# Kernel tuning notes

Measured on AMD Instinct MI355X. Metric: run time of the kernel, lower is better.

## Reference

```python
import jax, jax.numpy as jnp
import numpy as np

B, SQ, SK, D, H, DK, DV = 4, 2048, 2048, 1024, 16, 64, 64


def setup_inputs() -> dict:
    key = jax.random.key(0)
    ks = jax.random.split(key, 12)

    def xav(k, shape):
        fan_in, fan_out = shape[-2], shape[-1]
        lim = (6.0 / (fan_in + fan_out)) ** 0.5
        return jax.random.uniform(k, shape, jnp.float32, -lim, lim)

    return {
        "Q": jax.random.normal(ks[0], (B, SQ, D), jnp.float32),
        "K": jax.random.normal(ks[1], (B, SK, D), jnp.float32),
        "V": jax.random.normal(ks[2], (B, SK, D), jnp.float32),
        "padding_mask": jnp.zeros((B, 1, SK), jnp.bool_),
        "Wq": xav(ks[3], (H, D, DK)),
        "bq": jnp.zeros((H, DK), jnp.float32),
        "Wk": xav(ks[4], (H, D, DK)),
        "bk": jnp.zeros((H, DK), jnp.float32),
        "Wv": xav(ks[5], (H, D, DV)),
        "bv": jnp.zeros((H, DV), jnp.float32),
        "Wo": xav(ks[6], (H, DV, DV)),   # per-head Attention.linear
        "bo": jnp.zeros((H, DV), jnp.float32),
        "Wf": xav(ks[7], (H * DV, D)),   # final MultiHeadAttention.linear
        "bf": jnp.zeros((D,), jnp.float32),
    }


def reference(Q, K, V, padding_mask, Wq, bq, Wk, bk, Wv, bv, Wo, bo, Wf, bf):
    # Per-head projections, batched over heads instead of a python loop.
    q = jnp.einsum("bsd,hdk->bhsk", Q, Wq) + bq[:, None, :]  # [B,H,SQ,DK]
    k = jnp.einsum("bsd,hdk->bhsk", K, Wk) + bk[:, None, :]  # [B,H,SK,DK]
    v = jnp.einsum("bsd,hdv->bhsv", V, Wv) + bv[:, None, :]  # [B,H,SK,DV]

    scale = float(DK) ** 0.5
    w = jnp.einsum("bhqd,bhkd->bhqk", q, k) / scale           # [B,H,SQ,SK]

    causal = jnp.triu(jnp.ones((SQ, SK), jnp.bool_), 1)       # masking=True path
    w = jnp.where(causal[None, None], -jnp.inf, w)
    w = jnp.where(padding_mask[:, None, :, :], -jnp.inf, w)   # [B,1,1,SK]

    score = jnp.nan_to_num(jax.nn.softmax(w, axis=-1))        # nan_to_num as in torch
    # dropout p=0.0 -> identity
    ctx = jnp.einsum("bhqk,bhkv->bhqv", score, v)             # [B,H,SQ,DV]
    heads = jnp.einsum("bhqv,hvu->bhqu", ctx, Wo) + bo[:, None, :]
    concat = heads.transpose(0, 2, 1, 3).reshape(B, SQ, H * DV)
    return concat @ Wf + bf
```

## Files before the change

kernel.cpp:

```cpp
#include <hip/hip_runtime.h>

typedef unsigned short u16;
typedef unsigned int u32;
typedef __attribute__((ext_vector_type(8))) short short8;
typedef __attribute__((ext_vector_type(4))) float f32x4;

#define NEG (-1e30f)
#define SCL 0.180336880f

#define WS_WPQ   (0u)
#define WS_WPK   (2u<<20)
#define WS_WPV   (4u<<20)
#define WS_WBIG  (6u<<20)
#define WS_BC    (8u<<20)
#define WS_MB    ((8u<<20)+(1u<<16))
#define WS_MP    ((8u<<20)+(3u<<16))
#define WS_QB    (9u<<20)
#define WS_KB    (25u<<20)
#define WS_VB    (41u<<20)
#define WS_QP    (57u<<20)
#define WS_KP    (73u<<20)
#define WS_VP    (89u<<20)
#define WS_VT    (105u<<20)
#define WS_CTX   (121u<<20)

__device__ __forceinline__ u16 f2b(float f) {
    union { float f; unsigned u; } x; x.f = f;
    unsigned r = x.u + 0x7fffu + ((x.u >> 16) & 1u);
    return (u16)(r >> 16);
}

__device__ __forceinline__ u32 cvt_pk(float a, float b) {
    u32 r;
    asm("v_cvt_pk_bf16_f32 %0, %1, %2" : "=v"(r) : "v"(a), "v"(b));
    return r;
}

__device__ __forceinline__ void gload16(const void* g, void* lds) {
    __builtin_amdgcn_global_load_lds(
        (const __attribute__((address_space(1))) void*)g,
        (__attribute__((address_space(3))) void*)lds, 16, 0, 0);
}

__global__ __launch_bounds__(256) void conv_bf16(const float* __restrict__ in,
                                                 u16* __restrict__ out) {
    unsigned i = blockIdx.x * 256u + threadIdx.x;
    const float4* p = (const float4*)(in + (size_t)i * 8);
    float4 a = p[0], b = p[1];
    short8 o;
    o[0]=(short)f2b(a.x); o[1]=(short)f2b(a.y); o[2]=(short)f2b(a.z); o[3]=(short)f2b(a.w);
    o[4]=(short)f2b(b.x); o[5]=(short)f2b(b.y); o[6]=(short)f2b(b.z); o[7]=(short)f2b(b.w);
    *(short8*)(out + (size_t)i * 8) = o;
}

__global__ __launch_bounds__(256) void pack_qkv(const float* __restrict__ Wq,
                                                const float* __restrict__ Wk,
                                                const float* __restrict__ Wv,
                                                u16* __restrict__ pq,
                                                u16* __restrict__ pk,
                                                u16* __restrict__ pv) {
    __shared__ u16 T[64][68];
    const int dt = blockIdx.x, h = blockIdx.y;
    const int r = threadIdx.x >> 2, c0 = (threadIdx.x & 3) * 16;
    const float* srcs[3] = {Wq, Wk, Wv};
    u16* dsts[3] = {pq, pk, pv};
#pragma unroll
    for (int m = 0; m < 3; ++m) {
        const float* src = srcs[m] + (size_t)(h * 1024 + dt * 64 + r) * 64 + c0;
#pragma unroll
        for (int i4 = 0; i4 < 4; ++i4) {
            float4 x = *(const float4*)(src + i4 * 4);
            T[c0 + i4*4 + 0][r] = f2b(x.x);
            T[c0 + i4*4 + 1][r] = f2b(x.y);
            T[c0 + i4*4 + 2][r] = f2b(x.z);
            T[c0 + i4*4 + 3][r] = f2b(x.w);
        }
        __syncthreads();
        u16* dst = dsts[m] + (size_t)(h * 64 + r) * 1024 + dt * 64 + c0;
        short8 o0, o1;
#pragma unroll
        for (int i = 0; i < 8; ++i) { o0[i] = (short)T[r][c0 + i]; o1[i] = (short)T[r][c0 + 8 + i]; }
        *(short8*)dst = o0;
        *(short8*)(dst + 8) = o1;
        __syncthreads();
    }
}

__global__ __launch_bounds__(256) void make_wbig(const float* __restrict__ Wo,
                                                 const float* __restrict__ Wf,
                                                 u16* __restrict__ wbig) {
    __shared__ float WoL[64][64];
    const int ct = blockIdx.x, h = blockIdx.y;
    const int tid = threadIdx.x;
#pragma unroll
    for (int r = 0; r < 16; ++r) {
        int i = r * 256 + tid;
        WoL[i >> 6][i & 63] = Wo[h * 4096 + i];
    }
    __syncthreads();
    const int n = ct * 256 + tid;
    float wf[64];
#pragma unroll
    for (int u = 0; u < 64; ++u)
        wf[u] = Wf[(size_t)(h * 64 + u) * 1024 + n];
    u16* dst = wbig + (size_t)n * 1024 + h * 64;
    for (int vb = 0; vb < 64; vb += 8) {
        short8 o;
#pragma unroll
        for (int t = 0; t < 8; ++t) {
            int v = vb + t;
            float s = 0.f;
#pragma unroll
            for (int u4 = 0; u4 < 16; ++u4) {
                float4 w4 = *(const float4*)&WoL[v][u4 * 4];
                s += w4.x * wf[u4*4] + w4.y * wf[u4*4+1] + w4.z * wf[u4*4+2] + w4.w * wf[u4*4+3];
            }
            o[t] = (short)f2b(s);
        }
        *(short8*)(dst + vb) = o;
    }
}

__global__ __launch_bounds__(256) void make_bcomb(const float* __restrict__ bo,
                                                  const float* __restrict__ bf,
                                                  const float* __restrict__ Wf,
                                                  const unsigned char* __restrict__ pmask,
                                                  float* __restrict__ bc,
                                                  float* __restrict__ mbias,
                                                  int* __restrict__ mpart) {
    __shared__ float red[16][17];
    const int tx = threadIdx.x & 15, ty = threadIdx.x >> 4;
    const int n = blockIdx.x * 16 + tx;
    float s = 0.f;
#pragma unroll
    for (int i = 0; i < 64; ++i) {
        int x = ty * 64 + i;
        s += bo[x] * Wf[(size_t)x * 1024 + n];
    }
    red[ty][tx] = s;

    int t = blockIdx.x * 256 + threadIdx.x;
    int v = 0;
    if (t < 8192) {
        v = pmask[t] ? 1 : 0;
        mbias[t] = v ? NEG : 0.f;
    }
    int ba = __syncthreads_or(v);
    if (threadIdx.x == 0 && blockIdx.x < 32) mpart[blockIdx.x] = ba;

    if (ty == 0) {
        float tt = bf[n];
#pragma unroll
        for (int y = 0; y < 16; ++y) tt += red[y][tx];
        bc[n] = tt;
    }
}

__global__ __launch_bounds__(256) void vtrans(const u16* __restrict__ vp,
                                              u16* __restrict__ vt) {
    const int kvt = blockIdx.x, bh = blockIdx.y, b = bh >> 4, h = bh & 15;
    const int tid = threadIdx.x;
    __shared__ u16 T[64][72];
    {
        int kv_r = tid >> 2, dg = (tid & 3) * 16;
        const u16* src = vp + ((size_t)(b * 2048 + kvt * 64 + kv_r)) * 1024 + h * 64 + dg;
        short8 x0 = *(const short8*)src;
        short8 x1 = *(const short8*)(src + 8);
#pragma unroll
        for (int i = 0; i < 8; ++i) { T[dg + i][kv_r] = (u16)x0[i]; T[dg + 8 + i][kv_r] = (u16)x1[i]; }
    }
    __syncthreads();
    {
        int dv = tid >> 2, cg = (tid & 3) * 16;
        int swz = (dv & 7) << 3;
        u16* dst = vt + ((size_t)(bh * 64 + dv)) * 2048 + kvt * 64;
#pragma unroll
        for (int q = 0; q < 2; ++q) {
            int c0 = cg + q * 8;
            short8 y;
#pragma unroll
            for (int i = 0; i < 8; ++i) y[i] = (short)T[dv][c0 + i];
            *(short8*)(dst + (c0 ^ swz)) = y;
        }
    }
}

template <int OUT_BF16>
__global__ __launch_bounds__(256) void gemm_bf16(const u16* __restrict__ A,
                                                 const u16* __restrict__ Bt,
                                                 const float* __restrict__ bias,
                                                 void* __restrict__ Cv,
                                                 int M, int N, int K, float oscale) {
    __shared__ __align__(16) u16 As[2][128 * 64];
    __shared__ __align__(16) u16 Bs[2][128 * 64];
    const int tid = threadIdx.x;
    const int lane = tid & 63, w = tid >> 6;
    const int li = lane & 15, g = lane >> 4;
    const int bm = blockIdx.y * 128, bn = blockIdx.x * 128;
    const int wm = w >> 1, wn = w & 1;

    auto STAGE = [&](int buf, int k0) {
#pragma unroll
        for (int r = 0; r < 4; ++r) {
            int ch  = (r * 4 + w) * 64 + lane;
            int row = ch >> 3;
            int ck  = (ch & 7) ^ (row & 7);
            gload16(A  + (size_t)(bm + row) * K + k0 + ck * 8, (char*)(As[buf]) + (r * 4 + w) * 1024);
            gload16(Bt + (size_t)(bn + row) * K + k0 + ck * 8, (char*)(Bs[buf]) + (r * 4 + w) * 1024);
        }
    };

    f32x4 acc[4][4];
#pragma unroll
    for (int m = 0; m < 4; ++m)
#pragma unroll
        for (int n = 0; n < 4; ++n) acc[m][n] = (f32x4){0.f, 0.f, 0.f, 0.f};

    STAGE(0, 0);
    __syncthreads();
    int cur = 0;

    for (int k0 = 0; k0 < K; k0 += 64) {
        if (k0 + 64 < K) STAGE(cur ^ 1, k0 + 64);
#pragma unroll
        for (int kk = 0; kk < 2; ++kk) {
            short8 a[4], b[4];
#pragma unroll
            for (int m = 0; m < 4; ++m) {
                int row = wm * 64 + m * 16 + li;
                int c = (kk * 4 + g) ^ (row & 7);
                a[m] = *(const short8*)(As[cur] + row * 64 + c * 8);
            }
#pragma unroll
            for (int n = 0; n < 4; ++n) {
                int row = wn * 64 + n * 16 + li;
                int c = (kk * 4 + g) ^ (row & 7);
                b[n] = *(const short8*)(Bs[cur] + row * 64 + c * 8);
            }
#pragma unroll
            for (int m = 0; m < 4; ++m)
#pragma unroll
                for (int n = 0; n < 4; ++n)
                    acc[m][n] = __builtin_amdgcn_mfma_f32_16x16x32_bf16(a[m], b[n], acc[m][n], 0, 0, 0);
        }
        __syncthreads();
        cur ^= 1;
    }

#pragma unroll
    for (int n = 0; n < 4; ++n) {
        int col = bn + wn * 64 + n * 16 + li;
        float bv = bias[col];
#pragma unroll
        for (int m = 0; m < 4; ++m)
#pragma unroll
            for (int j = 0; j < 4; ++j) {
                int row = bm + wm * 64 + m * 16 + g * 4 + j;
                float v = (acc[m][n][j] + bv) * oscale;
                if (OUT_BF16) ((u16*)Cv)[(size_t)row * N + col] = f2b(v);
                else          ((float*)Cv)[(size_t)row * N + col] = v;
            }
    }
}

__global__ __launch_bounds__(256) void flash_attn(const u16* __restrict__ qp,
                                                  const u16* __restrict__ kp,
                                                  const u16* __restrict__ vt,
                                                  const float* __restrict__ mbias,
                                                  const int* __restrict__ mpart,
                                                  u16* __restrict__ ctx) {
    const int bh = blockIdx.x, b = bh >> 4, h = bh & 15;
    const int qt = 31 - blockIdx.y;
    const int tid = threadIdx.x, lane = tid & 63, w = tid >> 6;
    const int li = lane & 15, g = lane >> 4;

    __shared__ __align__(16) u16 Ks[2][64 * 64];
    __shared__ __align__(16) u16 Vs[2][64 * 64];
    __shared__ __align__(16) u16 Ps[64 * 64];

    auto STAGE = [&](int buf, int kt) {
#pragma unroll
        for (int r = 0; r < 2; ++r) {
            int ch  = (r * 4 + w) * 64 + lane;
            int row = ch >> 3, cc = ch & 7;
            int ck  = cc ^ (row & 7);
            gload16(kp + (size_t)(b * 2048 + kt * 64 + row) * 1024 + h * 64 + ck * 8,
                    (char*)(Ks[buf]) + (r * 4 + w) * 1024);
            gload16(vt + (size_t)(bh * 64 + row) * 2048 + kt * 64 + cc * 8,
                    (char*)(Vs[buf]) + (r * 4 + w) * 1024);
        }
    };

    STAGE(0, 0);
    const int rq = w * 16 + li;
    const u16* qg = qp + (size_t)(b * 2048 + qt * 64 + rq) * 1024 + h * 64;
    short8 aq0 = *(const short8*)(qg + g * 8);
    short8 aq1 = *(const short8*)(qg + 32 + g * 8);

    bool padded;
    {
        int a = 0;
#pragma unroll
        for (int i = 0; i < 8; ++i) a |= mpart[b * 8 + i];
        padded = (a != 0);
    }

    float m_i = NEG, l_i = 0.f;
    f32x4 o_acc[4];
#pragma unroll
    for (int n = 0; n < 4; ++n) o_acc[n] = (f32x4){0.f, 0.f, 0.f, 0.f};

    const float* mb = mbias + (size_t)b * 2048;
    const int swz = li & 7;

    __syncthreads();
    int cur = 0;

    auto TILE = [&](int kt, int buf, bool diag) {
        float mcv[16];
        if (padded) {
#pragma unroll
            for (int n = 0; n < 4; ++n)
                *(float4*)(mcv + n * 4) = *(const float4*)(mb + kt * 64 + n * 16 + g * 4);
        }

        f32x4 s[4];
#pragma unroll
        for (int n = 0; n < 4; ++n) s[n] = (f32x4){0.f, 0.f, 0.f, 0.f};
        __builtin_amdgcn_s_setprio(1);
#pragma unroll
        for (int kk = 0; kk < 2; ++kk) {
            short8 aq = kk ? aq1 : aq0;
#pragma unroll
            for (int n = 0; n < 4; ++n) {
                short8 bk = *(const short8*)(Ks[buf] + (n * 16 + li) * 64 + ((kk * 4 + g) ^ swz) * 8);
                s[n] = __builtin_amdgcn_mfma_f32_16x16x32_bf16(bk, aq, s[n], 0, 0, 0);
            }
        }
        __builtin_amdgcn_s_setprio(0);

        float rmax = NEG;
#pragma unroll
        for (int n = 0; n < 4; ++n)
#pragma unroll
            for (int j = 0; j < 4; ++j) {
                float v = s[n][j];
                if (padded) v += mcv[n * 4 + j];
                if (diag && (n * 16 + g * 4 + j) > rq) v = NEG;
                s[n][j] = v;
                rmax = fmaxf(rmax, v);
            }
        rmax = fmaxf(rmax, __shfl_xor(rmax, 16));
        rmax = fmaxf(rmax, __shfl_xor(rmax, 32));

        if (__any(rmax > m_i)) {
            float mn = fmaxf(m_i, rmax);
            float a  = exp2f(m_i - mn);
            m_i = mn;
            l_i *= a;
            float af[4];
#pragma unroll
            for (int j = 0; j < 4; ++j) af[j] = __shfl(a, g * 4 + j);
#pragma unroll
            for (int n = 0; n < 4; ++n)
#pragma unroll
                for (int j = 0; j < 4; ++j) o_acc[n][j] *= af[j];
        }

        float rs = 0.f;
#pragma unroll
        for (int n = 0; n < 4; ++n) {
            float p0 = exp2f(s[n][0] - m_i);
            float p1 = exp2f(s[n][1] - m_i);
            float p2 = exp2f(s[n][2] - m_i);
            float p3 = exp2f(s[n][3] - m_i);
            rs += (p0 + p1) + (p2 + p3);
            u32 lo = cvt_pk(p0, p1), hi = cvt_pk(p2, p3);
            int col = (n * 16 + g * 4) ^ (swz << 3);
            *(uint2*)(Ps + rq * 64 + col) = make_uint2(lo, hi);
        }
        rs += __shfl_xor(rs, 16);
        rs += __shfl_xor(rs, 32);
        l_i += rs;

        __builtin_amdgcn_s_setprio(1);
#pragma unroll
        for (int kk = 0; kk < 2; ++kk) {
            short8 pa = *(const short8*)(Ps + rq * 64 + ((kk * 4 + g) ^ swz) * 8);
#pragma unroll
            for (int n = 0; n < 4; ++n) {
                short8 vb = *(const short8*)(Vs[buf] + (n * 16 + li) * 64 + ((kk * 4 + g) ^ swz) * 8);
                o_acc[n] = __builtin_amdgcn_mfma_f32_16x16x32_bf16(pa, vb, o_acc[n], 0, 0, 0);
            }
        }
        __builtin_amdgcn_s_setprio(0);
    };

    for (int kt = 0; kt < qt; ++kt) {
        STAGE(cur ^ 1, kt + 1);
        TILE(kt, cur, false);
        __syncthreads();
        cur ^= 1;
    }
    TILE(qt, cur, true);

    float linv = 1.f / l_i;
    float lr[4];
#pragma unroll
    for (int j = 0; j < 4; ++j) lr[j] = __shfl(linv, g * 4 + j);
#pragma unroll
    for (int n = 0; n < 4; ++n)
#pragma unroll
        for (int j = 0; j < 4; ++j) {
            int rowq = qt * 64 + w * 16 + g * 4 + j;
            ctx[(size_t)(b * 2048 + rowq) * 1024 + h * 64 + n * 16 + li] = f2b(o_acc[n][j] * lr[j]);
        }
}

extern "C" void kernel_launch(void* const* d_in, const int* in_sizes, int n_in,
                              void* d_out, int out_size, void* d_ws, size_t ws_size,
                              hipStream_t stream) {
    const float* Q  = (const float*)d_in[0];
    const float* K  = (const float*)d_in[1];
    const float* V  = (const float*)d_in[2];
    const unsigned char* pmask = (const unsigned char*)d_in[3];
    const float* Wq = (const float*)d_in[4];
    const float* bq = (const float*)d_in[5];
    const float* Wk = (const float*)d_in[6];
    const float* bk = (const float*)d_in[7];
    const float* Wv = (const float*)d_in[8];
    const float* bv = (const float*)d_in[9];
    const float* Wo = (const float*)d_in[10];
    const float* bo = (const float*)d_in[11];
    const float* Wf = (const float*)d_in[12];
    const float* bf = (const float*)d_in[13];
    float* out = (float*)d_out;
    char*  ws  = (char*)d_ws;

    u16* WPQ = (u16*)(ws + WS_WPQ);  u16* WPK = (u16*)(ws + WS_WPK);
    u16* WPV = (u16*)(ws + WS_WPV);  u16* WBG = (u16*)(ws + WS_WBIG);
    float* BC = (float*)(ws + WS_BC);
    float* MB = (float*)(ws + WS_MB);
    int*   MP = (int*)(ws + WS_MP);
    u16* QB = (u16*)(ws + WS_QB);  u16* KB = (u16*)(ws + WS_KB);  u16* VB = (u16*)(ws + WS_VB);
    u16* QP = (u16*)(ws + WS_QP);  u16* KP = (u16*)(ws + WS_KP);  u16* VP = (u16*)(ws + WS_VP);
    u16* VT = (u16*)(ws + WS_VT);  u16* CTX = (u16*)(ws + WS_CTX);

    conv_bf16<<<4096, 256, 0, stream>>>(Q, QB);
    conv_bf16<<<4096, 256, 0, stream>>>(K, KB);
    conv_bf16<<<4096, 256, 0, stream>>>(V, VB);
    pack_qkv<<<dim3(16, 16), 256, 0, stream>>>(Wq, Wk, Wv, WPQ, WPK, WPV);
    make_wbig<<<dim3(4, 16), 256, 0, stream>>>(Wo, Wf, WBG);
    make_bcomb<<<64, 256, 0, stream>>>(bo, bf, Wf, pmask, BC, MB, MP);

    dim3 g1(8, 64);
    gemm_bf16<1><<<g1, 256, 0, stream>>>(QB, WPQ, bq, QP, 8192, 1024, 1024, SCL);
    gemm_bf16<1><<<g1, 256, 0, stream>>>(KB, WPK, bk, KP, 8192, 1024, 1024, 1.0f);
    gemm_bf16<1><<<g1, 256, 0, stream>>>(VB, WPV, bv, VP, 8192, 1024, 1024, 1.0f);

    vtrans<<<dim3(32, 64), 256, 0, stream>>>(VP, VT);

    flash_attn<<<dim3(64, 32), 256, 0, stream>>>(QP, KP, VT, MB, MP, CTX);

    gemm_bf16<0><<<g1, 256, 0, stream>>>(CTX, WBG, BC, out, 8192, 1024, 1024, 1.0f);
}
```

Measured before the change: 401.9 us.

## Fuse fp32-to-bf16 conversion into projection GEMMs and widen tiles to 128x256

Removes the three standalone conversion kernels: the projection GEMMs now read fp32 Q/K/V directly, convert them in registers and write bf16 into LDS. The GEMM becomes a 512-thread 128x256 tile with precomputed incremental source pointers and raised MFMA priority. The flash attention kernel gets incremental staging pointers and a different XOR swizzle for the P buffer to reduce LDS bank conflicts. The aim is to cut the extra HBM round trip for converted inputs and launch overhead. The cost is register-staged A loads that no longer go straight to LDS, and higher register and LDS use per block.

```diff
diff --git a/kernel.cpp b/kernel.cpp
--- a/kernel.cpp
+++ b/kernel.cpp
@@ -15,14 +15,11 @@
 #define WS_BC    (8u<<20)
 #define WS_MB    ((8u<<20)+(1u<<16))
 #define WS_MP    ((8u<<20)+(3u<<16))
-#define WS_QB    (9u<<20)
-#define WS_KB    (25u<<20)
-#define WS_VB    (41u<<20)
-#define WS_QP    (57u<<20)
-#define WS_KP    (73u<<20)
-#define WS_VP    (89u<<20)
-#define WS_VT    (105u<<20)
-#define WS_CTX   (121u<<20)
+#define WS_QP    (9u<<20)
+#define WS_KP    (25u<<20)
+#define WS_VP    (41u<<20)
+#define WS_VT    (57u<<20)
+#define WS_CTX   (73u<<20)
 
 __device__ __forceinline__ u16 f2b(float f) {
     union { float f; unsigned u; } x; x.f = f;
@@ -40,17 +37,6 @@
     __builtin_amdgcn_global_load_lds(
         (const __attribute__((address_space(1))) void*)g,
         (__attribute__((address_space(3))) void*)lds, 16, 0, 0);
-}
-
-__global__ __launch_bounds__(256) void conv_bf16(const float* __restrict__ in,
-                                                 u16* __restrict__ out) {
-    unsigned i = blockIdx.x * 256u + threadIdx.x;
-    const float4* p = (const float4*)(in + (size_t)i * 8);
-    float4 a = p[0], b = p[1];
-    short8 o;
-    o[0]=(short)f2b(a.x); o[1]=(short)f2b(a.y); o[2]=(short)f2b(a.z); o[3]=(short)f2b(a.w);
-    o[4]=(short)f2b(b.x); o[5]=(short)f2b(b.y); o[6]=(short)f2b(b.z); o[7]=(short)f2b(b.w);
-    *(short8*)(out + (size_t)i * 8) = o;
 }
 
 __global__ __launch_bounds__(256) void pack_qkv(const float* __restrict__ Wq,
@@ -185,30 +171,76 @@
     }
 }
 
-template <int OUT_BF16>
-__global__ __launch_bounds__(256) void gemm_bf16(const u16* __restrict__ A,
-                                                 const u16* __restrict__ Bt,
-                                                 const float* __restrict__ bias,
-                                                 void* __restrict__ Cv,
-                                                 int M, int N, int K, float oscale) {
+template <int A_F32, int OUT_BF16>
+__global__ __launch_bounds__(512) void gemm_bn256(const void* __restrict__ Av,
+                                                  const u16* __restrict__ Bt,
+                                                  const float* __restrict__ bias,
+                                                  void* __restrict__ Cv,
+                                                  int M, int N, int K, float oscale) {
     __shared__ __align__(16) u16 As[2][128 * 64];
-    __shared__ __align__(16) u16 Bs[2][128 * 64];
+    __shared__ __align__(16) u16 Bs[2][256 * 64];
     const int tid = threadIdx.x;
     const int lane = tid & 63, w = tid >> 6;
     const int li = lane & 15, g = lane >> 4;
-    const int bm = blockIdx.y * 128, bn = blockIdx.x * 128;
-    const int wm = w >> 1, wn = w & 1;
-
-    auto STAGE = [&](int buf, int k0) {
+    const int bm = blockIdx.y * 128, bn = blockIdx.x * 256;
+    const int wm = w >> 2, wn = w & 3;
+
+    const u16* bsrc[4];
+    int bdst[4];
+#pragma unroll
+    for (int r = 0; r < 4; ++r) {
+        int ch = (r * 8 + w) * 64 + lane;
+        int row = ch >> 3;
+        int ck = (ch & 7) ^ (row & 7);
+        bsrc[r] = Bt + (size_t)(bn + row) * K + ck * 8;
+        bdst[r] = (r * 8 + w) * 1024;
+    }
+    const float* afsrc[2];
+    const u16*   a16src[2];
+    int aoff[2], adst[2];
+#pragma unroll
+    for (int r = 0; r < 2; ++r) {
+        int ch = (r * 8 + w) * 64 + lane;
+        int row = ch >> 3;
+        int ck = (ch & 7) ^ (row & 7);
+        if (A_F32) afsrc[r] = (const float*)Av + (size_t)(bm + row) * K + ck * 8;
+        else       a16src[r] = (const u16*)Av + (size_t)(bm + row) * K + ck * 8;
+        aoff[r] = ch * 8;
+        adst[r] = (r * 8 + w) * 1024;
+    }
+
+    auto STAGE_B = [&](int buf) {
 #pragma unroll
         for (int r = 0; r < 4; ++r) {
-            int ch  = (r * 4 + w) * 64 + lane;
-            int row = ch >> 3;
-            int ck  = (ch & 7) ^ (row & 7);
-            gload16(A  + (size_t)(bm + row) * K + k0 + ck * 8, (char*)(As[buf]) + (r * 4 + w) * 1024);
-            gload16(Bt + (size_t)(bn + row) * K + k0 + ck * 8, (char*)(Bs[buf]) + (r * 4 + w) * 1024);
+            gload16(bsrc[r], (char*)(Bs[buf]) + bdst[r]);
+            bsrc[r] += 64;
         }
     };
+    auto STAGE_A16 = [&](int buf) {
+#pragma unroll
+        for (int r = 0; r < 2; ++r) {
+            gload16(a16src[r], (char*)(As[buf]) + adst[r]);
+            a16src[r] += 64;
+        }
+    };
+    auto LOAD_A = [&](float4 fa[2][2]) {
+#pragma unroll
+        for (int r = 0; r < 2; ++r) {
+            fa[r][0] = *(const float4*)afsrc[r];
+            fa[r][1] = *(const float4*)(afsrc[r] + 4);
+            afsrc[r] += 64;
+        }
+    };
+    auto WRITE_A = [&](int buf, float4 fa[2][2]) {
+#pragma unroll
+        for (int r = 0; r < 2; ++r) {
+            u32 q0 = cvt_pk(fa[r][0].x, fa[r][0].y);
+            u32 q1 = cvt_pk(fa[r][0].z, fa[r][0].w);
+            u32 q2 = cvt_pk(fa[r][1].x, fa[r][1].y);
+            u32 q3 = cvt_pk(fa[r][1].z, fa[r][1].w);
+            *(uint4*)(As[buf] + aoff[r]) = make_uint4(q0, q1, q2, q3);
+        }
+    };
 
     f32x4 acc[4][4];
 #pragma unroll
@@ -216,12 +248,23 @@
 #pragma unroll
         for (int n = 0; n < 4; ++n) acc[m][n] = (f32x4){0.f, 0.f, 0.f, 0.f};
 
-    STAGE(0, 0);
+    {
+        float4 fa[2][2];
+        if (A_F32) LOAD_A(fa); else STAGE_A16(0);
+        STAGE_B(0);
+        if (A_F32) WRITE_A(0, fa);
+    }
     __syncthreads();
     int cur = 0;
 
     for (int k0 = 0; k0 < K; k0 += 64) {
-        if (k0 + 64 < K) STAGE(cur ^ 1, k0 + 64);
+        const bool more = (k0 + 64 < K);
+        float4 fa[2][2];
+        if (more) {
+            if (A_F32) LOAD_A(fa); else STAGE_A16(cur ^ 1);
+            STAGE_B(cur ^ 1);
+        }
+        __builtin_amdgcn_s_setprio(1);
 #pragma unroll
         for (int kk = 0; kk < 2; ++kk) {
             short8 a[4], b[4];
@@ -243,6 +286,8 @@
                 for (int n = 0; n < 4; ++n)
                     acc[m][n] = __builtin_amdgcn_mfma_f32_16x16x32_bf16(a[m], b[n], acc[m][n], 0, 0, 0);
         }
+        __builtin_amdgcn_s_setprio(0);
+        if (more && A_F32) WRITE_A(cur ^ 1, fa);
         __syncthreads();
         cur ^= 1;
     }
@@ -278,20 +323,31 @@
     __shared__ __align__(16) u16 Vs[2][64 * 64];
     __shared__ __align__(16) u16 Ps[64 * 64];
 
-    auto STAGE = [&](int buf, int kt) {
+    const u16 *ksrc[2], *vsrc[2];
+    int sdst[2];
+#pragma unroll
+    for (int r = 0; r < 2; ++r) {
+        int ch = (r * 4 + w) * 64 + lane;
+        int row = ch >> 3, cc = ch & 7;
+        int ck = cc ^ (row & 7);
+        ksrc[r] = kp + (size_t)(b * 2048 + row) * 1024 + h * 64 + ck * 8;
+        vsrc[r] = vt + (size_t)(bh * 64 + row) * 2048 + cc * 8;
+        sdst[r] = (r * 4 + w) * 1024;
+    }
+    auto STAGE = [&](int buf) {
 #pragma unroll
         for (int r = 0; r < 2; ++r) {
-            int ch  = (r * 4 + w) * 64 + lane;
-            int row = ch >> 3, cc = ch & 7;
-            int ck  = cc ^ (row & 7);
-            gload16(kp + (size_t)(b * 2048 + kt * 64 + row) * 1024 + h * 64 + ck * 8,
-                    (char*)(Ks[buf]) + (r * 4 + w) * 1024);
-            gload16(vt + (size_t)(bh * 64 + row) * 2048 + kt * 64 + cc * 8,
-                    (char*)(Vs[buf]) + (r * 4 + w) * 1024);
+            gload16(ksrc[r], (char*)(Ks[buf]) + sdst[r]);
+            gload16(vsrc[r], (char*)(Vs[buf]) + sdst[r]);
+            ksrc[r] += 64 * 1024;
+            vsrc[r] += 64;
         }
     };
 
-    STAGE(0, 0);
+#pragma unroll
+    for (int r = 0; r < 2; ++r) {  }
+
+    STAGE(0);
     const int rq = w * 16 + li;
     const u16* qg = qp + (size_t)(b * 2048 + qt * 64 + rq) * 1024 + h * 64;
     short8 aq0 = *(const short8*)(qg + g * 8);
@@ -311,7 +367,8 @@
     for (int n = 0; n < 4; ++n) o_acc[n] = (f32x4){0.f, 0.f, 0.f, 0.f};
 
     const float* mb = mbias + (size_t)b * 2048;
-    const int swz = li & 7;
+    const int swz  = li & 7;
+    const int pswz = (li & 7) ^ (li >> 3);
 
     __syncthreads();
     int cur = 0;
@@ -376,7 +433,7 @@
             float p3 = exp2f(s[n][3] - m_i);
             rs += (p0 + p1) + (p2 + p3);
             u32 lo = cvt_pk(p0, p1), hi = cvt_pk(p2, p3);
-            int col = (n * 16 + g * 4) ^ (swz << 3);
+            int col = (n * 16 + g * 4) ^ (pswz << 3);
             *(uint2*)(Ps + rq * 64 + col) = make_uint2(lo, hi);
         }
         rs += __shfl_xor(rs, 16);
@@ -386,7 +443,7 @@
         __builtin_amdgcn_s_setprio(1);
 #pragma unroll
         for (int kk = 0; kk < 2; ++kk) {
-            short8 pa = *(const short8*)(Ps + rq * 64 + ((kk * 4 + g) ^ swz) * 8);
+            short8 pa = *(const short8*)(Ps + rq * 64 + ((kk * 4 + g) ^ pswz) * 8);
 #pragma unroll
             for (int n = 0; n < 4; ++n) {
                 short8 vb = *(const short8*)(Vs[buf] + (n * 16 + li) * 64 + ((kk * 4 + g) ^ swz) * 8);
@@ -397,7 +454,7 @@
     };
 
     for (int kt = 0; kt < qt; ++kt) {
-        STAGE(cur ^ 1, kt + 1);
+        STAGE(cur ^ 1);
         TILE(kt, cur, false);
         __syncthreads();
         cur ^= 1;
@@ -442,25 +499,21 @@
     float* BC = (float*)(ws + WS_BC);
     float* MB = (float*)(ws + WS_MB);
     int*   MP = (int*)(ws + WS_MP);
-    u16* QB = (u16*)(ws + WS_QB);  u16* KB = (u16*)(ws + WS_KB);  u16* VB = (u16*)(ws + WS_VB);
     u16* QP = (u16*)(ws + WS_QP);  u16* KP = (u16*)(ws + WS_KP);  u16* VP = (u16*)(ws + WS_VP);
     u16* VT = (u16*)(ws + WS_VT);  u16* CTX = (u16*)(ws + WS_CTX);
 
-    conv_bf16<<<4096, 256, 0, stream>>>(Q, QB);
-    conv_bf16<<<4096, 256, 0, stream>>>(K, KB);
-    conv_bf16<<<4096, 256, 0, stream>>>(V, VB);
     pack_qkv<<<dim3(16, 16), 256, 0, stream>>>(Wq, Wk, Wv, WPQ, WPK, WPV);
     make_wbig<<<dim3(4, 16), 256, 0, stream>>>(Wo, Wf, WBG);
     make_bcomb<<<64, 256, 0, stream>>>(bo, bf, Wf, pmask, BC, MB, MP);
 
-    dim3 g1(8, 64);
-    gemm_bf16<1><<<g1, 256, 0, stream>>>(QB, WPQ, bq, QP, 8192, 1024, 1024, SCL);
-    gemm_bf16<1><<<g1, 256, 0, stream>>>(KB, WPK, bk, KP, 8192, 1024, 1024, 1.0f);
-    gemm_bf16<1><<<g1, 256, 0, stream>>>(VB, WPV, bv, VP, 8192, 1024, 1024, 1.0f);
+    dim3 gp(4, 64);
+    gemm_bn256<1, 1><<<gp, 512, 0, stream>>>(Q, WPQ, bq, QP, 8192, 1024, 1024, SCL);
+    gemm_bn256<1, 1><<<gp, 512, 0, stream>>>(K, WPK, bk, KP, 8192, 1024, 1024, 1.0f);
+    gemm_bn256<1, 1><<<gp, 512, 0, stream>>>(V, WPV, bv, VP, 8192, 1024, 1024, 1.0f);
 
     vtrans<<<dim3(32, 64), 256, 0, stream>>>(VP, VT);
 
     flash_attn<<<dim3(64, 32), 256, 0, stream>>>(QP, KP, VT, MB, MP, CTX);
 
-    gemm_bf16<0><<<g1, 256, 0, stream>>>(CTX, WBG, BC, out, 8192, 1024, 1024, 1.0f);
-}
+    gemm_bn256<0, 0><<<gp, 512, 0, stream>>>(CTX, WBG, BC, out, 8192, 1024, 1024, 1.0f);
+}
```

Result: slower. 423.0 us (+5.2%).
